# Kernel optimization log

Measured on AMD Instinct MI355X. Metric: run time of the kernel, lower is better.

The kernel has to match this reference:

```python
import jax, jax.numpy as jnp
import numpy as np
from jax import lax

# Config (matches init_kwargs / ModelCfg.__post_init__)
B, L = 2, 1024
D, E, N, D_DELTA, D_CONV, V, N_LAYERS = 768, 1536, 16, 48, 4, 50280, 2


def setup_inputs() -> dict:
    key = jax.random.key(0)
    ks = jax.random.split(key, 16)
    s = 0.02
    inp = {
        "tokens": jax.random.randint(ks[0], (B, L), 0, V),
        "embedding": jax.random.normal(ks[1], (V, D), jnp.float32) * s,
        "norm_w": jnp.ones((N_LAYERS, D), jnp.float32),
        "skip_w": jax.random.normal(ks[2], (N_LAYERS, E, D), jnp.float32) * s,
        "in_w": jax.random.normal(ks[3], (N_LAYERS, E, D), jnp.float32) * s,
        "conv_w": jax.random.normal(ks[4], (N_LAYERS, E, 1, D_CONV), jnp.float32) * 0.1,
        "conv_b": jax.random.normal(ks[5], (N_LAYERS, E), jnp.float32) * s,
        "Wd1": jax.random.normal(ks[6], (N_LAYERS, D_DELTA, E), jnp.float32) * s,
        "Wd2_w": jax.random.normal(ks[7], (N_LAYERS, E, D_DELTA), jnp.float32) * s,
        "Wd2_b": jax.random.normal(ks[8], (N_LAYERS, E), jnp.float32) * s,
        "WB": jax.random.normal(ks[9], (N_LAYERS, N, E), jnp.float32) * s,
        "WC": jax.random.normal(ks[10], (N_LAYERS, N, E), jnp.float32) * s,
        "A_log": jax.random.normal(ks[11], (N_LAYERS, E, N), jnp.float32) * 0.5,
        "W_D": jnp.ones((N_LAYERS, E), jnp.float32),
        "out_w": jax.random.normal(ks[12], (N_LAYERS, D, E), jnp.float32) * s,
        "final_norm_w": jnp.ones((D,), jnp.float32),
        "lm_head_w": jax.random.normal(ks[13], (V, D), jnp.float32) * s,
    }
    return inp


def rmsnorm(x, w, eps=1e-5):
    return x * lax.rsqrt(jnp.mean(x * x, axis=-1, keepdims=True) + eps) * w


def mamba_block(resid, nw, skw, inw, cw, cb, wd1, wd2w, wd2b, wb, wc, a_log, wd, ow):
    x = rmsnorm(resid, nw)                      # [B,L,D]
    skip = x @ skw.T                            # [B,L,E]
    xi = x @ inw.T                              # [B,L,E]
    # depthwise causal conv1d (left pad D_CONV-1 == torch pad + slice [:L])
    xc = lax.conv_general_dilated(
        xi.transpose(0, 2, 1), cw, window_strides=(1,),
        padding=[(D_CONV - 1, 0)], feature_group_count=E,
        dimension_numbers=("NCH", "OIH", "NCH"))
    x = jax.nn.silu((xc + cb[None, :, None]).transpose(0, 2, 1))  # [B,L,E]

    A = -jnp.exp(a_log)                                            # [E,N]
    delta = jax.nn.softplus((x @ wd1.T) @ wd2w.T + wd2b)           # [B,L,E]
    Bm = x @ wb.T                                                  # [B,L,N]
    Cm = x @ wc.T                                                  # [B,L,N]
    dA = jnp.exp(delta[..., None] * A)                             # [B,L,E,N]
    dBx = delta[..., None] * Bm[:, :, None, :] * x[..., None]      # [B,L,E,N]

    def step(h, t):
        dA_t, dBx_t, C_t = t
        h = dA_t * h + dBx_t                                       # [B,E,N]
        y = jnp.einsum("ben,bn->be", h, C_t)
        return h, y

    h0 = jnp.zeros((B, E, N), x.dtype)
    _, ys = lax.scan(step, h0, (dA.transpose(1, 0, 2, 3),
                                dBx.transpose(1, 0, 2, 3),
                                Cm.transpose(1, 0, 2)))
    y = ys.transpose(1, 0, 2)                                      # [B,L,E]
    y = (y + x * wd) * jax.nn.silu(skip)
    return resid + y @ ow.T


def reference(tokens, embedding, norm_w, skip_w, in_w, conv_w, conv_b, Wd1,
              Wd2_w, Wd2_b, WB, WC, A_log, W_D, out_w, final_norm_w, lm_head_w):
    resid = embedding[tokens]                                      # [B,L,D]
    for i in range(N_LAYERS):
        resid = mamba_block(resid, norm_w[i], skip_w[i], in_w[i], conv_w[i],
                            conv_b[i], Wd1[i], Wd2_w[i], Wd2_b[i], WB[i],
                            WC[i], A_log[i], W_D[i], out_w[i])
    resid = rmsnorm(resid, final_norm_w)
    logits = resid @ lm_head_w.T                                   # [B,L,V]
    return logits
```

## Files before the change

### kernel.cpp

```cpp
#include <hip/hip_runtime.h>
#include <hip/hip_bf16.h>

#define BB     2
#define LL     1024
#define BL     (BB*LL)
#define BDIM   768
#define EDIM   1536
#define NST    16
#define DDELTA 48
#define DDPAD  64
#define DCONV  4
#define VOCAB  50280
#define NLAYERS 2

#define CCH    16
#define TCH    (LL/CCH)
#define BEN    (BB*EDIM*NST)

typedef __hip_bfloat16 bf16;
typedef short short8 __attribute__((ext_vector_type(8)));
typedef float floatx4 __attribute__((ext_vector_type(4)));

static __device__ __forceinline__ bf16  f2bf(float v){ return __float2bfloat16(v); }
static __device__ __forceinline__ short f2bs(float v){
  bf16 b = f2bf(v); return *reinterpret_cast<short*>(&b);
}
static __device__ __forceinline__ short8 pack_bf16(float4 a, float4 b){
  short8 r;
  r[0]=f2bs(a.x); r[1]=f2bs(a.y); r[2]=f2bs(a.z); r[3]=f2bs(a.w);
  r[4]=f2bs(b.x); r[5]=f2bs(b.y); r[6]=f2bs(b.z); r[7]=f2bs(b.w);
  return r;
}

typedef const __attribute__((address_space(1))) unsigned int gu32;
typedef __attribute__((address_space(3))) unsigned int lu32;
static __device__ __forceinline__ void glds16(const bf16* g, bf16* l) {
  __builtin_amdgcn_global_load_lds((gu32*)g, (lu32*)l, 16, 0, 0);
}

__global__ void k_embed(const int* __restrict__ tok, const float* __restrict__ emb,
                        float* __restrict__ resid) {
  int idx = blockIdx.x*256 + threadIdx.x;
  int bl = idx / BDIM, d = idx % BDIM;
  resid[idx] = emb[(size_t)tok[bl]*BDIM + d];
}

__global__ __launch_bounds__(256) void k_rmsnorm(const float* __restrict__ resid,
                        const float* __restrict__ w, bf16* __restrict__ out) {
  int m = blockIdx.x, tid = threadIdx.x;
  const float* row = resid + (size_t)m*BDIM;
  float ss = 0.f;
  for (int d = tid; d < BDIM; d += 256) { float v = row[d]; ss += v*v; }
  for (int off = 32; off; off >>= 1) ss += __shfl_down(ss, off);
  __shared__ float red[4];
  if ((tid & 63) == 0) red[tid>>6] = ss;
  __syncthreads();
  float rstd = rsqrtf((red[0]+red[1]+red[2]+red[3]) / (float)BDIM + 1e-5f);
  for (int d = tid; d < BDIM; d += 256)
    out[(size_t)m*BDIM + d] = f2bf(row[d]*rstd*w[d]);
}

template<bool OUT_BF16>
__global__ __launch_bounds__(256) void k_gemm(const bf16* __restrict__ A,
      const float* __restrict__ W, void* __restrict__ Cp, int N, int K) {
  __shared__ alignas(16) bf16 As[2][128*32];
  __shared__ alignas(16) bf16 Bs[2][128*32];
  const int nwg = gridDim.x * gridDim.y;
  const int orig = blockIdx.y * gridDim.x + blockIdx.x;
  const int qq = nwg >> 3, rr = nwg & 7;
  const int xcd = orig & 7, sub = orig >> 3;
  const int logical = (xcd < rr ? xcd*(qq+1) : rr*(qq+1) + (xcd-rr)*qq) + sub;
  const int by = logical % gridDim.y;
  const int bx = logical / gridDim.y;
  const int m0 = by * 128, n0 = bx * 128;

  const int tid = threadIdx.x, lane = tid & 63, wave = tid >> 6;
  const int wm = (wave >> 1) * 64, wn = (wave & 1) * 64;
  const int mr = lane & 15, q = lane >> 4;
  floatx4 acc[4][4] = {};

  const int sr = lane >> 2, ch = lane & 3;
  const int wbase = wave * 16;
  const int sA = (sr >> 1) & 3;
  const bf16* Ar0 = A + (size_t)(m0 + wbase + sr)*K      + (ch ^ sA)*8;
  const bf16* Ar1 = A + (size_t)(m0 + 64 + wbase + sr)*K + (ch ^ sA)*8;

  const int wrow = tid >> 2, wc = tid & 3;
  const int sW = (wrow >> 1) & 3;
  int gn0 = n0 + wrow;      if (gn0 >= N) gn0 = N - 1;
  int gn1 = n0 + 64 + wrow; if (gn1 >= N) gn1 = N - 1;
  const float* Wp0 = W + (size_t)gn0*K + (wc ^ sW)*8;
  const float* Wp1 = W + (size_t)gn1*K + (wc ^ sW)*8;

  const int nt = K >> 5;
  float4 wA0, wA1, wB0, wB1;

  glds16(Ar0, &As[0][wbase*32]);
  glds16(Ar1, &As[0][(64+wbase)*32]);
  wA0 = *(const float4*)(Wp0);  wA1 = *(const float4*)(Wp0 + 4);
  wB0 = *(const float4*)(Wp1);  wB1 = *(const float4*)(Wp1 + 4);

  const int swq = (q ^ ((mr >> 1) & 3)) * 8;

  for (int t = 0; t < nt; ++t) {
    const int cur = t & 1;
    asm volatile("s_waitcnt vmcnt(0)" ::: "memory");
    *reinterpret_cast<short8*>(&Bs[cur][wrow*32      + wc*8]) = pack_bf16(wA0, wA1);
    *reinterpret_cast<short8*>(&Bs[cur][(64+wrow)*32 + wc*8]) = pack_bf16(wB0, wB1);
    asm volatile("s_waitcnt lgkmcnt(0)" ::: "memory");
    __builtin_amdgcn_s_barrier();
    if (t + 1 < nt) {
      const int k0 = (t + 1) * 32;
      glds16(Ar0 + k0, &As[cur^1][wbase*32]);
      glds16(Ar1 + k0, &As[cur^1][(64+wbase)*32]);
      wA0 = *(const float4*)(Wp0 + k0);  wA1 = *(const float4*)(Wp0 + k0 + 4);
      wB0 = *(const float4*)(Wp1 + k0);  wB1 = *(const float4*)(Wp1 + k0 + 4);
    }
    asm volatile("" ::: "memory");
    short8 af[4], bfr[4];
    #pragma unroll
    for (int i = 0; i < 4; i++)
      af[i]  = *reinterpret_cast<const short8*>(&As[cur][(wm + i*16 + mr)*32 + swq]);
    #pragma unroll
    for (int j = 0; j < 4; j++)
      bfr[j] = *reinterpret_cast<const short8*>(&Bs[cur][(wn + j*16 + mr)*32 + swq]);
    #pragma unroll
    for (int i = 0; i < 4; i++)
      #pragma unroll
      for (int j = 0; j < 4; j++)
        acc[i][j] = __builtin_amdgcn_mfma_f32_16x16x32_bf16(af[i], bfr[j], acc[i][j], 0, 0, 0);
  }
  #pragma unroll
  for (int i = 0; i < 4; i++)
    #pragma unroll
    for (int j = 0; j < 4; j++)
      #pragma unroll
      for (int rg = 0; rg < 4; rg++) {
        int m = m0 + wm + i*16 + q*4 + rg;
        int n = n0 + wn + j*16 + mr;
        if (n < N) {
          float v = acc[i][j][rg];
          if (OUT_BF16) ((bf16*)Cp)[(size_t)m*N + n] = f2bf(v);
          else          ((float*)Cp)[(size_t)m*N + n] = v;
        }
      }
}

__global__ void k_conv(const float* __restrict__ xi, const float* __restrict__ cw,
                       const float* __restrict__ cb, float* __restrict__ xc) {
  int idx = blockIdx.x*256 + threadIdx.x;
  int e = idx % EDIM, bl = idx / EDIM, l = bl % LL;
  float acc = cb[e];
  #pragma unroll
  for (int k = 0; k < DCONV; k++) {
    int ls = l - (DCONV-1) + k;
    if (ls >= 0) acc += xi[(size_t)(bl + ls - l)*EDIM + e] * cw[e*DCONV + k];
  }
  xc[idx] = acc / (1.f + expf(-acc));
}

__global__ __launch_bounds__(256) void k_d1(const float* __restrict__ xc,
      const float* __restrict__ wd1, bf16* __restrict__ d1) {
  int m = blockIdx.x, tid = threadIdx.x;
  __shared__ float xrow[EDIM];
  for (int k = tid; k < EDIM; k += 256) xrow[k] = xc[(size_t)m*EDIM + k];
  __syncthreads();
  int wave = tid >> 6, lane = tid & 63;
  for (int n = wave; n < DDPAD; n += 4) {
    float s = 0.f;
    if (n < DDELTA) {
      const float* wr = wd1 + (size_t)n*EDIM;
      for (int k = lane; k < EDIM; k += 64) s += xrow[k]*wr[k];
      for (int off = 32; off; off >>= 1) s += __shfl_down(s, off);
    }
    if (lane == 0) d1[(size_t)m*DDPAD + n] = f2bf(s);
  }
}

__global__ void k_padw32(const float* __restrict__ wsrc, float* __restrict__ wp) {
  int idx = blockIdx.x*256 + threadIdx.x;
  int e = idx >> 6, cc = idx & 63;
  wp[idx] = (cc < DDELTA) ? wsrc[(size_t)e*DDELTA + cc] : 0.f;
}

__global__ void k_softplus(float* __restrict__ d, const float* __restrict__ b) {
  int idx = blockIdx.x*256 + threadIdx.x;
  int e = idx % EDIM;
  float v = d[idx] + b[e];
  d[idx] = fmaxf(v, 0.f) + log1pf(expf(-fabsf(v)));
}

__global__ __launch_bounds__(256) void k_bc(const float* __restrict__ xc,
    const float* __restrict__ wb, const float* __restrict__ wc,
    float* __restrict__ Bm, float* __restrict__ Cm) {
  int m = blockIdx.x, tid = threadIdx.x;
  __shared__ float xrow[EDIM];
  for (int k = tid; k < EDIM; k += 256) xrow[k] = xc[(size_t)m*EDIM + k];
  __syncthreads();
  int wave = tid >> 6, lane = tid & 63;
  for (int n = wave; n < 32; n += 4) {
    const float* wr = (n < NST) ? wb + (size_t)n*EDIM : wc + (size_t)(n-NST)*EDIM;
    float s = 0.f;
    for (int k = lane; k < EDIM; k += 64) s += xrow[k]*wr[k];
    for (int off = 32; off; off >>= 1) s += __shfl_down(s, off);
    if (lane == 0) {
      if (n < NST) Bm[(size_t)m*NST + n]       = s;
      else         Cm[(size_t)m*NST + (n-NST)] = s;
    }
  }
}


__global__ __launch_bounds__(256) void k_scan1(const float* __restrict__ delta,
    const float* __restrict__ xc, const float* __restrict__ Bm,
    const float* __restrict__ a_log, float* __restrict__ Pbuf,
    float* __restrict__ Hbuf) {
  int tid = threadIdx.x;
  int n = tid & 15, el = tid >> 4;
  int bx = blockIdx.x;
  int et = bx % (EDIM/16); bx /= (EDIM/16);
  int c = bx % CCH, b = bx / CCH;
  int e = et*16 + el;
  float Aen = -__expf(a_log[(size_t)e*NST + n]);
  const float* dp = delta + ((size_t)b*LL + (size_t)c*TCH)*EDIM + e;
  const float* xp = xc    + ((size_t)b*LL + (size_t)c*TCH)*EDIM + e;
  const float* bp = Bm    + ((size_t)b*LL + (size_t)c*TCH)*NST + n;
  float h = 0.f, p = 1.f;
  #pragma unroll 4
  for (int t = 0; t < TCH; t++) {
    float dl = dp[(size_t)t*EDIM];
    float xv = xp[(size_t)t*EDIM];
    float bv = bp[t*NST];
    float a = __expf(dl*Aen);
    h = a*h + dl*bv*xv;
    p *= a;
  }
  size_t ben = ((size_t)b*EDIM + e)*NST + n;
  Pbuf[(size_t)c*BEN + ben] = p;
  Hbuf[(size_t)c*BEN + ben] = h;
}

__global__ __launch_bounds__(256) void k_scanfix(const float* __restrict__ Pbuf,
    const float* __restrict__ Hbuf, float* __restrict__ Hin) {
  int ben = blockIdx.x*256 + threadIdx.x;
  float h = 0.f;
  #pragma unroll
  for (int c = 0; c < CCH; c++) {
    Hin[(size_t)c*BEN + ben] = h;
    h = Pbuf[(size_t)c*BEN + ben]*h + Hbuf[(size_t)c*BEN + ben];
  }
}

__global__ __launch_bounds__(256) void k_scan2(const float* __restrict__ delta,
    const float* __restrict__ xc, const float* __restrict__ Bm,
    const float* __restrict__ Cm, const float* __restrict__ a_log,
    const float* __restrict__ Hin, float* __restrict__ y) {
  int tid = threadIdx.x;
  int n = tid & 15, el = tid >> 4;
  int bx = blockIdx.x;
  int et = bx % (EDIM/16); bx /= (EDIM/16);
  int c = bx % CCH, b = bx / CCH;
  int e = et*16 + el;
  float Aen = -__expf(a_log[(size_t)e*NST + n]);
  const float* dp = delta + ((size_t)b*LL + (size_t)c*TCH)*EDIM + e;
  const float* xp = xc    + ((size_t)b*LL + (size_t)c*TCH)*EDIM + e;
  const float* bp = Bm    + ((size_t)b*LL + (size_t)c*TCH)*NST + n;
  const float* cp = Cm    + ((size_t)b*LL + (size_t)c*TCH)*NST + n;
  float* yp = y + ((size_t)b*LL + (size_t)c*TCH)*EDIM + e;
  size_t ben = ((size_t)b*EDIM + e)*NST + n;
  float h = Hin[(size_t)c*BEN + ben];
  #pragma unroll 4
  for (int t = 0; t < TCH; t++) {
    float dl = dp[(size_t)t*EDIM];
    float xv = xp[(size_t)t*EDIM];
    float bv = bp[t*NST];
    float cv = cp[t*NST];
    h = __expf(dl*Aen)*h + dl*bv*xv;
    float p = h*cv;
    p += __shfl_xor(p, 1); p += __shfl_xor(p, 2);
    p += __shfl_xor(p, 4); p += __shfl_xor(p, 8);
    if (n == 0) yp[(size_t)t*EDIM] = p;
  }
}

__global__ void k_ymix(const float* __restrict__ y, const float* __restrict__ xc,
    const float* __restrict__ skip, const float* __restrict__ wd, bf16* __restrict__ y2) {
  int idx = blockIdx.x*256 + threadIdx.x;
  int e = idx % EDIM;
  float s = skip[idx];
  y2[idx] = f2bf((y[idx] + xc[idx]*wd[e]) * (s / (1.f + expf(-s))));
}

__global__ void k_add(float* __restrict__ resid, const float* __restrict__ d) {
  int idx = blockIdx.x*256 + threadIdx.x;
  resid[idx] += d[idx];
}

extern "C" void kernel_launch(void* const* d_in, const int* in_sizes, int n_in,
                              void* d_out, int out_size, void* d_ws, size_t ws_size,
                              hipStream_t stream) {
  const int*   tokens = (const int*)  d_in[0];
  const float* emb    = (const float*)d_in[1];
  const float* norm_w = (const float*)d_in[2];
  const float* skip_w = (const float*)d_in[3];
  const float* in_w   = (const float*)d_in[4];
  const float* conv_w = (const float*)d_in[5];
  const float* conv_b = (const float*)d_in[6];
  const float* Wd1    = (const float*)d_in[7];
  const float* Wd2w   = (const float*)d_in[8];
  const float* Wd2b   = (const float*)d_in[9];
  const float* WBw    = (const float*)d_in[10];
  const float* WCw    = (const float*)d_in[11];
  const float* A_log  = (const float*)d_in[12];
  const float* W_D    = (const float*)d_in[13];
  const float* out_w  = (const float*)d_in[14];
  const float* fnw    = (const float*)d_in[15];
  const float* lm_w   = (const float*)d_in[16];
  float* out = (float*)d_out;

  char* wsp = (char*)d_ws;
  auto alloc = [&](size_t bytes) { char* p = wsp; wsp += (bytes + 255) & ~(size_t)255; return p; };
  float* resid = (float*)alloc((size_t)BL*BDIM*4);
  bf16*  xn    = (bf16*) alloc((size_t)BL*BDIM*2);
  float* skip  = (float*)alloc((size_t)BL*EDIM*4);
  float* xi    = (float*)alloc((size_t)BL*EDIM*4);
  float* xc    = (float*)alloc((size_t)BL*EDIM*4);
  float* dlt   = (float*)alloc((size_t)BL*EDIM*4);
  bf16*  d1    = (bf16*) alloc((size_t)BL*DDPAD*2);
  float* w2p32 = (float*)alloc((size_t)EDIM*DDPAD*4);
  float* Bm    = (float*)alloc((size_t)BL*NST*4);
  float* Cm    = (float*)alloc((size_t)BL*NST*4);
  bf16*  y2    = (bf16*) alloc((size_t)BL*EDIM*2);
  float* Pbuf  = (float*)alloc((size_t)CCH*BEN*4);
  float* Hbuf  = (float*)alloc((size_t)CCH*BEN*4);
  float* Hin   = (float*)alloc((size_t)CCH*BEN*4);

  dim3 blk(256);
  const int scanGrid = BB*CCH*(EDIM/16);
  k_embed<<<BL*BDIM/256, blk, 0, stream>>>(tokens, emb, resid);
  for (int l = 0; l < NLAYERS; l++) {
    k_rmsnorm<<<BL, blk, 0, stream>>>(resid, norm_w + (size_t)l*BDIM, xn);

    k_gemm<false><<<dim3(EDIM/128, BL/128), blk, 0, stream>>>(
        xn, skip_w + (size_t)l*EDIM*BDIM, skip, EDIM, BDIM);
    k_gemm<false><<<dim3(EDIM/128, BL/128), blk, 0, stream>>>(
        xn, in_w + (size_t)l*EDIM*BDIM, xi, EDIM, BDIM);

    k_conv<<<BL*EDIM/256, blk, 0, stream>>>(
        xi, conv_w + (size_t)l*EDIM*DCONV, conv_b + (size_t)l*EDIM, xc);
    k_d1<<<BL, blk, 0, stream>>>(xc, Wd1 + (size_t)l*DDELTA*EDIM, d1);
    k_padw32<<<EDIM*DDPAD/256, blk, 0, stream>>>(Wd2w + (size_t)l*EDIM*DDELTA, w2p32);
    k_gemm<false><<<dim3(EDIM/128, BL/128), blk, 0, stream>>>(d1, w2p32, dlt, EDIM, DDPAD);
    k_softplus<<<BL*EDIM/256, blk, 0, stream>>>(dlt, Wd2b + (size_t)l*EDIM);
    k_bc<<<BL, blk, 0, stream>>>(xc, WBw + (size_t)l*NST*EDIM, WCw + (size_t)l*NST*EDIM, Bm, Cm);

    k_scan1<<<scanGrid, blk, 0, stream>>>(dlt, xc, Bm,
        A_log + (size_t)l*EDIM*NST, Pbuf, Hbuf);
    k_scanfix<<<BEN/256, blk, 0, stream>>>(Pbuf, Hbuf, Hin);
    k_scan2<<<scanGrid, blk, 0, stream>>>(dlt, xc, Bm, Cm,
        A_log + (size_t)l*EDIM*NST, Hin, xi);

    k_ymix<<<BL*EDIM/256, blk, 0, stream>>>(xi, xc, skip, W_D + (size_t)l*EDIM, y2);

    k_gemm<false><<<dim3(BDIM/128, BL/128), blk, 0, stream>>>(
        y2, out_w + (size_t)l*BDIM*EDIM, dlt, BDIM, EDIM);
    k_add<<<BL*BDIM/256, blk, 0, stream>>>(resid, dlt);
  }
  k_rmsnorm<<<BL, blk, 0, stream>>>(resid, fnw, xn);
  k_gemm<false><<<dim3((VOCAB+127)/128, BL/128), blk, 0, stream>>>(
      xn, lm_w, out, VOCAB, BDIM);
}
```

Before: 1.694 ms.

## Fuse softplus, ymix and residual add into neighbors; drop GEMM double buffering

Softplus with bias moves into the delta GEMM epilogue, the y/skip gating moves into scan2, and the residual add moves into the out-projection GEMM epilogue. This removes three elementwise kernels and their global memory round trips. The GEMM main loop also goes from a double-buffered software pipeline to a single-buffered loop with two barriers per K step. That exposes load latency in every GEMM, including the large lm_head GEMM that dominates runtime.

```diff
diff --git a/kernel.cpp b/kernel.cpp
--- a/kernel.cpp
+++ b/kernel.cpp
@@ -60,11 +60,12 @@
     out[(size_t)m*BDIM + d] = f2bf(row[d]*rstd*w[d]);
 }
 
-template<bool OUT_BF16>
+template<int MODE>
 __global__ __launch_bounds__(256) void k_gemm(const bf16* __restrict__ A,
-      const float* __restrict__ W, void* __restrict__ Cp, int N, int K) {
-  __shared__ alignas(16) bf16 As[2][128*32];
-  __shared__ alignas(16) bf16 Bs[2][128*32];
+      const float* __restrict__ W, void* __restrict__ Cp,
+      const float* __restrict__ bias, int N, int K) {
+  __shared__ alignas(16) bf16 As[128*32];
+  __shared__ alignas(16) bf16 Bs[128*32];
   const int nwg = gridDim.x * gridDim.y;
   const int orig = blockIdx.y * gridDim.x + blockIdx.x;
   const int qq = nwg >> 3, rr = nwg & 7;
@@ -92,38 +93,27 @@
   const float* Wp0 = W + (size_t)gn0*K + (wc ^ sW)*8;
   const float* Wp1 = W + (size_t)gn1*K + (wc ^ sW)*8;
 
-  const int nt = K >> 5;
-  float4 wA0, wA1, wB0, wB1;
-
-  glds16(Ar0, &As[0][wbase*32]);
-  glds16(Ar1, &As[0][(64+wbase)*32]);
-  wA0 = *(const float4*)(Wp0);  wA1 = *(const float4*)(Wp0 + 4);
-  wB0 = *(const float4*)(Wp1);  wB1 = *(const float4*)(Wp1 + 4);
-
   const int swq = (q ^ ((mr >> 1) & 3)) * 8;
 
-  for (int t = 0; t < nt; ++t) {
-    const int cur = t & 1;
+  for (int k0 = 0; k0 < K; k0 += 32) {
+    float4 w00 = *(const float4*)(Wp0 + k0);
+    float4 w01 = *(const float4*)(Wp0 + k0 + 4);
+    float4 w10 = *(const float4*)(Wp1 + k0);
+    float4 w11 = *(const float4*)(Wp1 + k0 + 4);
+    __syncthreads();
+    glds16(Ar0 + k0, As + wbase*32);
+    glds16(Ar1 + k0, As + (64 + wbase)*32);
+    *reinterpret_cast<short8*>(&Bs[wrow*32      + wc*8]) = pack_bf16(w00, w01);
+    *reinterpret_cast<short8*>(&Bs[(64+wrow)*32 + wc*8]) = pack_bf16(w10, w11);
     asm volatile("s_waitcnt vmcnt(0)" ::: "memory");
-    *reinterpret_cast<short8*>(&Bs[cur][wrow*32      + wc*8]) = pack_bf16(wA0, wA1);
-    *reinterpret_cast<short8*>(&Bs[cur][(64+wrow)*32 + wc*8]) = pack_bf16(wB0, wB1);
-    asm volatile("s_waitcnt lgkmcnt(0)" ::: "memory");
-    __builtin_amdgcn_s_barrier();
-    if (t + 1 < nt) {
-      const int k0 = (t + 1) * 32;
-      glds16(Ar0 + k0, &As[cur^1][wbase*32]);
-      glds16(Ar1 + k0, &As[cur^1][(64+wbase)*32]);
-      wA0 = *(const float4*)(Wp0 + k0);  wA1 = *(const float4*)(Wp0 + k0 + 4);
-      wB0 = *(const float4*)(Wp1 + k0);  wB1 = *(const float4*)(Wp1 + k0 + 4);
-    }
-    asm volatile("" ::: "memory");
+    __syncthreads();
     short8 af[4], bfr[4];
     #pragma unroll
     for (int i = 0; i < 4; i++)
-      af[i]  = *reinterpret_cast<const short8*>(&As[cur][(wm + i*16 + mr)*32 + swq]);
+      af[i]  = *reinterpret_cast<const short8*>(&As[(wm + i*16 + mr)*32 + swq]);
     #pragma unroll
     for (int j = 0; j < 4; j++)
-      bfr[j] = *reinterpret_cast<const short8*>(&Bs[cur][(wn + j*16 + mr)*32 + swq]);
+      bfr[j] = *reinterpret_cast<const short8*>(&Bs[(wn + j*16 + mr)*32 + swq]);
     #pragma unroll
     for (int i = 0; i < 4; i++)
       #pragma unroll
@@ -140,8 +130,16 @@
         int n = n0 + wn + j*16 + mr;
         if (n < N) {
           float v = acc[i][j][rg];
-          if (OUT_BF16) ((bf16*)Cp)[(size_t)m*N + n] = f2bf(v);
-          else          ((float*)Cp)[(size_t)m*N + n] = v;
+          if (MODE == 0) {
+            ((float*)Cp)[(size_t)m*N + n] = v;
+          } else if (MODE == 1) {
+            float w = v + bias[n];
+            ((float*)Cp)[(size_t)m*N + n] =
+                fmaxf(w, 0.f) + log1pf(expf(-fabsf(w)));
+          } else {
+            float* p = (float*)Cp + (size_t)m*N + n;
+            *p += v;
+          }
         }
       }
 }
@@ -181,13 +179,6 @@
   int idx = blockIdx.x*256 + threadIdx.x;
   int e = idx >> 6, cc = idx & 63;
   wp[idx] = (cc < DDELTA) ? wsrc[(size_t)e*DDELTA + cc] : 0.f;
-}
-
-__global__ void k_softplus(float* __restrict__ d, const float* __restrict__ b) {
-  int idx = blockIdx.x*256 + threadIdx.x;
-  int e = idx % EDIM;
-  float v = d[idx] + b[e];
-  d[idx] = fmaxf(v, 0.f) + log1pf(expf(-fabsf(v)));
 }
 
 __global__ __launch_bounds__(256) void k_bc(const float* __restrict__ xc,
@@ -254,7 +245,8 @@
 __global__ __launch_bounds__(256) void k_scan2(const float* __restrict__ delta,
     const float* __restrict__ xc, const float* __restrict__ Bm,
     const float* __restrict__ Cm, const float* __restrict__ a_log,
-    const float* __restrict__ Hin, float* __restrict__ y) {
+    const float* __restrict__ Hin, const float* __restrict__ skip,
+    const float* __restrict__ wd, bf16* __restrict__ y2) {
   int tid = threadIdx.x;
   int n = tid & 15, el = tid >> 4;
   int bx = blockIdx.x;
@@ -266,9 +258,11 @@
   const float* xp = xc    + ((size_t)b*LL + (size_t)c*TCH)*EDIM + e;
   const float* bp = Bm    + ((size_t)b*LL + (size_t)c*TCH)*NST + n;
   const float* cp = Cm    + ((size_t)b*LL + (size_t)c*TCH)*NST + n;
-  float* yp = y + ((size_t)b*LL + (size_t)c*TCH)*EDIM + e;
+  const float* sp = skip  + ((size_t)b*LL + (size_t)c*TCH)*EDIM + e;
+  bf16* yp = y2 + ((size_t)b*LL + (size_t)c*TCH)*EDIM + e;
   size_t ben = ((size_t)b*EDIM + e)*NST + n;
   float h = Hin[(size_t)c*BEN + ben];
+  float wdv = wd[e];
   #pragma unroll 4
   for (int t = 0; t < TCH; t++) {
     float dl = dp[(size_t)t*EDIM];
@@ -279,21 +273,12 @@
     float p = h*cv;
     p += __shfl_xor(p, 1); p += __shfl_xor(p, 2);
     p += __shfl_xor(p, 4); p += __shfl_xor(p, 8);
-    if (n == 0) yp[(size_t)t*EDIM] = p;
-  }
-}
-
-__global__ void k_ymix(const float* __restrict__ y, const float* __restrict__ xc,
-    const float* __restrict__ skip, const float* __restrict__ wd, bf16* __restrict__ y2) {
-  int idx = blockIdx.x*256 + threadIdx.x;
-  int e = idx % EDIM;
-  float s = skip[idx];
-  y2[idx] = f2bf((y[idx] + xc[idx]*wd[e]) * (s / (1.f + expf(-s))));
-}
-
-__global__ void k_add(float* __restrict__ resid, const float* __restrict__ d) {
-  int idx = blockIdx.x*256 + threadIdx.x;
-  resid[idx] += d[idx];
+    if (n == 0) {
+      float sv = sp[(size_t)t*EDIM];
+      float yv = (p + xv*wdv) * (sv / (1.f + expf(-sv)));
+      yp[(size_t)t*EDIM] = f2bf(yv);
+    }
+  }
 }
 
 extern "C" void kernel_launch(void* const* d_in, const int* in_sizes, int n_in,
@@ -341,32 +326,29 @@
   for (int l = 0; l < NLAYERS; l++) {
     k_rmsnorm<<<BL, blk, 0, stream>>>(resid, norm_w + (size_t)l*BDIM, xn);
 
-    k_gemm<false><<<dim3(EDIM/128, BL/128), blk, 0, stream>>>(
-        xn, skip_w + (size_t)l*EDIM*BDIM, skip, EDIM, BDIM);
-    k_gemm<false><<<dim3(EDIM/128, BL/128), blk, 0, stream>>>(
-        xn, in_w + (size_t)l*EDIM*BDIM, xi, EDIM, BDIM);
+    k_gemm<0><<<dim3(EDIM/128, BL/128), blk, 0, stream>>>(
+        xn, skip_w + (size_t)l*EDIM*BDIM, skip, nullptr, EDIM, BDIM);
+    k_gemm<0><<<dim3(EDIM/128, BL/128), blk, 0, stream>>>(
+        xn, in_w + (size_t)l*EDIM*BDIM, xi, nullptr, EDIM, BDIM);
 
     k_conv<<<BL*EDIM/256, blk, 0, stream>>>(
         xi, conv_w + (size_t)l*EDIM*DCONV, conv_b + (size_t)l*EDIM, xc);
     k_d1<<<BL, blk, 0, stream>>>(xc, Wd1 + (size_t)l*DDELTA*EDIM, d1);
     k_padw32<<<EDIM*DDPAD/256, blk, 0, stream>>>(Wd2w + (size_t)l*EDIM*DDELTA, w2p32);
-    k_gemm<false><<<dim3(EDIM/128, BL/128), blk, 0, stream>>>(d1, w2p32, dlt, EDIM, DDPAD);
-    k_softplus<<<BL*EDIM/256, blk, 0, stream>>>(dlt, Wd2b + (size_t)l*EDIM);
+    k_gemm<1><<<dim3(EDIM/128, BL/128), blk, 0, stream>>>(
+        d1, w2p32, dlt, Wd2b + (size_t)l*EDIM, EDIM, DDPAD);
     k_bc<<<BL, blk, 0, stream>>>(xc, WBw + (size_t)l*NST*EDIM, WCw + (size_t)l*NST*EDIM, Bm, Cm);
 
     k_scan1<<<scanGrid, blk, 0, stream>>>(dlt, xc, Bm,
         A_log + (size_t)l*EDIM*NST, Pbuf, Hbuf);
     k_scanfix<<<BEN/256, blk, 0, stream>>>(Pbuf, Hbuf, Hin);
     k_scan2<<<scanGrid, blk, 0, stream>>>(dlt, xc, Bm, Cm,
-        A_log + (size_t)l*EDIM*NST, Hin, xi);
-
-    k_ymix<<<BL*EDIM/256, blk, 0, stream>>>(xi, xc, skip, W_D + (size_t)l*EDIM, y2);
-
-    k_gemm<false><<<dim3(BDIM/128, BL/128), blk, 0, stream>>>(
-        y2, out_w + (size_t)l*BDIM*EDIM, dlt, BDIM, EDIM);
-    k_add<<<BL*BDIM/256, blk, 0, stream>>>(resid, dlt);
+        A_log + (size_t)l*EDIM*NST, Hin, skip, W_D + (size_t)l*EDIM, y2);
+
+    k_gemm<2><<<dim3(BDIM/128, BL/128), blk, 0, stream>>>(
+        y2, out_w + (size_t)l*BDIM*EDIM, resid, nullptr, BDIM, EDIM);
   }
   k_rmsnorm<<<BL, blk, 0, stream>>>(resid, fnw, xn);
-  k_gemm<false><<<dim3((VOCAB+127)/128, BL/128), blk, 0, stream>>>(
-      xn, lm_w, out, VOCAB, BDIM);
-}
+  k_gemm<0><<<dim3((VOCAB+127)/128, BL/128), blk, 0, stream>>>(
+      xn, lm_w, out, nullptr, VOCAB, BDIM);
+}
```

After: 1.827 ms. 7.9% more time.
